# Performance work log

Measured on AMD Instinct MI355X. Metric: run time of the kernel, lower is better.

Reference implementation:

```python
import jax, jax.numpy as jnp
import numpy as np

N_NODES = 50000
IN_F = 512
OUT_F = 512
N_EDGES = 1600000
DROP_P = 0.5
NEG_SLOPE = 0.01  # torch LeakyReLU default


def leaky_relu(x):
    return jnp.where(x >= 0, x, NEG_SLOPE * x)


def setup_inputs() -> dict:
    key = jax.random.key(0)
    k1, k2, k3, k4, k5, k6 = jax.random.split(key, 6)
    x = jax.random.normal(k1, (N_NODES, IN_F), dtype=jnp.float32)
    W = jax.random.normal(k2, (OUT_F, IN_F), dtype=jnp.float32) * (1.0 / np.sqrt(IN_F))
    # inverted dropout mask: bernoulli(keep)/keep, keep = 1 - p
    keep = 1.0 - DROP_P
    drop_mask = (jax.random.uniform(k3, (N_NODES, IN_F)) < keep).astype(jnp.float32) / keep
    adj_vals = jax.random.uniform(k4, (N_EDGES,), dtype=jnp.float32)
    adj_rows = jax.random.randint(k5, (N_EDGES,), 0, N_NODES, dtype=jnp.int32)
    adj_cols = jax.random.randint(k6, (N_EDGES,), 0, N_NODES, dtype=jnp.int32)
    return {"x": x, "W": W, "drop_mask": drop_mask, "adj_vals": adj_vals,
            "adj_rows": adj_rows, "adj_cols": adj_cols}


def reference(x, W, drop_mask, adj_vals, adj_rows, adj_cols):
    # support = Linear(dropout(x)); Linear weight is [out, in] (torch convention)
    support = jnp.einsum('ni,oi->no', x * drop_mask, W)  # [N, out]
    h = leaky_relu(support)
    # sparse adj @ h: out[r] += v * h[c]
    msgs = adj_vals[:, None] * h[adj_cols]               # [E, out]
    agg = jax.ops.segment_sum(msgs, adj_rows, num_segments=N_NODES)
    return leaky_relu(agg)
```

## Files before the change

kernel.cpp:

```cpp
#include <hip/hip_runtime.h>

#define NROWS 50000
#define NFEAT 512
#define NEDGE 1600000
#define SLOPE 0.01f

typedef unsigned short u16;
typedef __attribute__((ext_vector_type(8))) short short8;
typedef __attribute__((ext_vector_type(4))) float f32x4;
typedef __attribute__((ext_vector_type(8))) unsigned short u16x8;

__device__ __forceinline__ u16 f2bf(float f) {
  unsigned u = __float_as_uint(f);
  u += 0x7fffu + ((u >> 16) & 1u);
  return (u16)(u >> 16);
}
__device__ __forceinline__ float lrelu(float v) { return v >= 0.f ? v : SLOPE * v; }

__device__ __forceinline__ void gload_lds16(const u16* g, u16* l) {
  __builtin_amdgcn_global_load_lds((const __attribute__((address_space(1))) void*)g,
                                   (__attribute__((address_space(3))) void*)l, 16, 0, 0);
}

__global__ void prep_kernel(const float* __restrict__ x, const float* __restrict__ m,
                            u16* __restrict__ xd, const float* __restrict__ w,
                            u16* __restrict__ wb, const int* __restrict__ rows,
                            int* __restrict__ counts) {
  const int stride = gridDim.x * blockDim.x;
  const int tid0 = blockIdx.x * blockDim.x + threadIdx.x;
  for (int i = tid0; i < (NROWS * NFEAT) / 8; i += stride) {
    size_t b = (size_t)i * 2;
    float4 a0 = ((const float4*)x)[b], a1 = ((const float4*)x)[b + 1];
    float4 m0 = ((const float4*)m)[b], m1 = ((const float4*)m)[b + 1];
    u16x8 o;
    o[0] = f2bf(a0.x * m0.x); o[1] = f2bf(a0.y * m0.y);
    o[2] = f2bf(a0.z * m0.z); o[3] = f2bf(a0.w * m0.w);
    o[4] = f2bf(a1.x * m1.x); o[5] = f2bf(a1.y * m1.y);
    o[6] = f2bf(a1.z * m1.z); o[7] = f2bf(a1.w * m1.w);
    *(u16x8*)(xd + (size_t)i * 8) = o;
  }
  for (int i = tid0; i < (NFEAT * NFEAT) / 8; i += stride) {
    size_t b = (size_t)i * 2;
    float4 a0 = ((const float4*)w)[b], a1 = ((const float4*)w)[b + 1];
    u16x8 o;
    o[0] = f2bf(a0.x); o[1] = f2bf(a0.y); o[2] = f2bf(a0.z); o[3] = f2bf(a0.w);
    o[4] = f2bf(a1.x); o[5] = f2bf(a1.y); o[6] = f2bf(a1.z); o[7] = f2bf(a1.w);
    *(u16x8*)(wb + (size_t)i * 8) = o;
  }
  for (int i = tid0; i < NEDGE / 4; i += stride) {
    int4 r4 = ((const int4*)rows)[i];
    atomicAdd(&counts[r4.x], 1);
    atomicAdd(&counts[r4.y], 1);
    atomicAdd(&counts[r4.z], 1);
    atomicAdd(&counts[r4.w], 1);
  }
}

__global__ void scan_kernel(const int* __restrict__ counts, int* __restrict__ offs) {
  __shared__ int wpre[17];
  const int t = threadIdx.x;
  const int lane = t & 63, w = t >> 6;
  const int beg = t * 64;
  int4 c4[16];
  int s = 0;
  if (beg < NROWS) {
#pragma unroll
    for (int g = 0; g < 16; ++g) {
      int idx = beg + g * 4;
      if (idx < NROWS) {
        c4[g] = ((const int4*)counts)[idx >> 2];
        s += c4[g].x + c4[g].y + c4[g].z + c4[g].w;
      }
    }
  }
  int inc = s;
#pragma unroll
  for (int d = 1; d < 64; d <<= 1) {
    int u = __shfl_up(inc, d);
    if (lane >= d) inc += u;
  }
  if (lane == 63) wpre[w + 1] = inc;
  __syncthreads();
  if (t == 0) {
    wpre[0] = 0;
    for (int i = 1; i <= 16; ++i) wpre[i] += wpre[i - 1];
    offs[NROWS] = wpre[16];
  }
  __syncthreads();
  int run = wpre[w] + inc - s;
  if (beg < NROWS) {
#pragma unroll
    for (int g = 0; g < 16; ++g) {
      int idx = beg + g * 4;
      if (idx < NROWS) {
        int4 o;
        o.x = run; run += c4[g].x;
        o.y = run; run += c4[g].y;
        o.z = run; run += c4[g].z;
        o.w = run; run += c4[g].w;
        ((int4*)offs)[idx >> 2] = o;
      }
    }
  }
}

__global__ void scatter_kernel(const float* __restrict__ vals, const int* __restrict__ rows,
                               const int* __restrict__ cols, const int* __restrict__ offs,
                               int* __restrict__ cursor, int2* __restrict__ svc) {
  int e0 = (blockIdx.x * blockDim.x + threadIdx.x) * 4;
  if (e0 >= NEDGE) return;
  int4 r4 = *(const int4*)(rows + e0);
  int4 c4 = *(const int4*)(cols + e0);
  float4 v4 = *(const float4*)(vals + e0);
  int rr[4] = {r4.x, r4.y, r4.z, r4.w};
  int cc[4] = {c4.x, c4.y, c4.z, c4.w};
  float vv[4] = {v4.x, v4.y, v4.z, v4.w};
#pragma unroll
  for (int j = 0; j < 4; ++j) {
    int p = offs[rr[j]] + atomicAdd(&cursor[rr[j]], 1);
    int2 q;
    q.x = __float_as_int(vv[j]);
    q.y = cc[j];
    svc[p] = q;
  }
}

__global__ __launch_bounds__(256) void gemm_kernel(const u16* __restrict__ xd,
                                                   const u16* __restrict__ wb,
                                                   unsigned char* __restrict__ hq,
                                                   float* __restrict__ scaleg) {
  __shared__ __align__(16) u16 lAB[2 * 128 * 64];
  __shared__ float wmax[2][128];
  __shared__ float rinv[128];
  u16* lA = lAB;
  u16* lB = lAB + 128 * 64;
  const int tid = threadIdx.x;
  const int lane = tid & 63;
  const int wid = tid >> 6;
  const int wm = wid >> 1, wn = wid & 1;
  const int bx = blockIdx.x;
  const int tm = bx >> 2;
  const int tn = bx & 3;
  const long rowBase = (long)tm * 128;

  f32x4 acc[4][4] = {};

  const int sl8 = lane >> 3;
  const int scol = ((lane & 7) ^ sl8) * 8;
  const int rsel = lane & 15, kgrp = (lane >> 4) * 8;

  for (int k0 = 0; k0 < 512; k0 += 64) {
    __syncthreads();
#pragma unroll
    for (int c = 0; c < 4; ++c) {
      int rbase = wid * 32 + c * 8;
      long gr = rowBase + rbase + sl8;
      if (gr > NROWS - 1) gr = NROWS - 1;
      gload_lds16(xd + gr * 512 + k0 + scol, lA + rbase * 64);
      gload_lds16(wb + ((long)tn * 128 + rbase + sl8) * 512 + k0 + scol, lB + rbase * 64);
    }
    __syncthreads();
    short8 a[4][2], b[4][2];
#pragma unroll
    for (int m = 0; m < 4; ++m) {
      int ar = wm * 64 + m * 16 + rsel;
      const u16* base = lA + ar * 64;
      int sw = (ar & 7) << 3;
      a[m][0] = *(const short8*)(base + (kgrp ^ sw));
      a[m][1] = *(const short8*)(base + ((32 + kgrp) ^ sw));
    }
#pragma unroll
    for (int n = 0; n < 4; ++n) {
      int br = wn * 64 + n * 16 + rsel;
      const u16* base = lB + br * 64;
      int sw = (br & 7) << 3;
      b[n][0] = *(const short8*)(base + (kgrp ^ sw));
      b[n][1] = *(const short8*)(base + ((32 + kgrp) ^ sw));
    }
#pragma unroll
    for (int kk = 0; kk < 2; ++kk)
#pragma unroll
      for (int m = 0; m < 4; ++m)
#pragma unroll
        for (int n = 0; n < 4; ++n)
          acc[m][n] = __builtin_amdgcn_mfma_f32_16x16x32_bf16(a[m][kk], b[n][kk], acc[m][n], 0, 0, 0);
  }

  const int crow = (lane >> 4) * 4;
  const int ccol = lane & 15;

  float pm[4][4];
#pragma unroll
  for (int m = 0; m < 4; ++m)
#pragma unroll
    for (int r2 = 0; r2 < 4; ++r2) {
      float mx = 0.f;
#pragma unroll
      for (int n = 0; n < 4; ++n) mx = fmaxf(mx, fabsf(lrelu(acc[m][n][r2])));
      pm[m][r2] = mx;
    }
#pragma unroll
  for (int d = 1; d < 16; d <<= 1)
#pragma unroll
    for (int m = 0; m < 4; ++m)
#pragma unroll
      for (int r2 = 0; r2 < 4; ++r2) pm[m][r2] = fmaxf(pm[m][r2], __shfl_xor(pm[m][r2], d));
  if ((lane & 15) == 0) {
#pragma unroll
    for (int m = 0; m < 4; ++m)
#pragma unroll
      for (int r2 = 0; r2 < 4; ++r2) wmax[wn][wm * 64 + m * 16 + crow + r2] = pm[m][r2];
  }
  __syncthreads();
  if (tid < 128) {
    float rm = fmaxf(wmax[0][tid], wmax[1][tid]);
    float s = rm > 0.f ? rm * (1.f / 127.f) : 1.f;
    rinv[tid] = rm > 0.f ? 127.f / rm : 0.f;
    long gr = rowBase + tid;
    if (gr < NROWS) scaleg[gr * 4 + tn] = s;
  }
  __syncthreads();

  unsigned char* lT = (unsigned char*)lAB;
#pragma unroll
  for (int m = 0; m < 4; ++m) {
    int row0 = wm * 64 + m * 16 + crow;
    float ri0 = rinv[row0], ri1 = rinv[row0 + 1], ri2 = rinv[row0 + 2], ri3 = rinv[row0 + 3];
#pragma unroll
    for (int n = 0; n < 4; ++n) {
      int col = wn * 64 + n * 16 + ccol;
      float q0 = rintf(lrelu(acc[m][n][0]) * ri0);
      float q1 = rintf(lrelu(acc[m][n][1]) * ri1);
      float q2 = rintf(lrelu(acc[m][n][2]) * ri2);
      float q3 = rintf(lrelu(acc[m][n][3]) * ri3);
      int i0 = min(127, max(-127, (int)q0));
      int i1 = min(127, max(-127, (int)q1));
      int i2 = min(127, max(-127, (int)q2));
      int i3 = min(127, max(-127, (int)q3));
      unsigned pk = (i0 & 0xff) | ((i1 & 0xff) << 8) | ((i2 & 0xff) << 16) | ((i3 & 0xff) << 24);
#pragma unroll
      for (int r2 = 0; r2 < 4; ++r2) {
        int row = row0 + r2;
        lT[row * 128 + (col ^ ((row & 7) << 4))] = (unsigned char)(pk >> (8 * r2));
      }
    }
  }
  __syncthreads();
  {
    const int row = tid >> 1, seg = tid & 1;
    long gr = rowBase + row;
    if (gr < NROWS) {
      unsigned char* dst = hq + gr * 512 + tn * 128;
#pragma unroll
      for (int j = 0; j < 4; ++j) {
        int s = seg * 4 + j;
        int4 vv = *(const int4*)(lT + row * 128 + ((s ^ (row & 7)) << 4));
        *(int4*)(dst + s * 16) = vv;
      }
    }
  }
}

__global__ __launch_bounds__(256) void aggregate_kernel(const unsigned char* __restrict__ hq,
                                                        const float* __restrict__ scaleg,
                                                        const int2* __restrict__ svc,
                                                        const int* __restrict__ offs,
                                                        float* __restrict__ out) {
  const int lane = threadIdx.x & 63;
  const int wid = threadIdx.x >> 6;
  const int p = blockIdx.x / 12500;
  const int r = (blockIdx.x % 12500) * 4 + wid;
  if (r >= NROWS) return;
  const int beg = offs[r], end = offs[r + 1];
  const int grp = p * 2 + (lane >> 5);
  float a0 = 0.f, a1 = 0.f, a2 = 0.f, a3 = 0.f;
  const unsigned char* hp = hq + p * 256 + lane * 4;
  int2 cb[8], nb[8];
  const int ng = (end - beg) >> 3;
  if (ng > 0) {
#pragma unroll
    for (int k = 0; k < 8; ++k) cb[k] = svc[beg + k];
  }
  for (int g = 0; g < ng; ++g) {
    if (g + 1 < ng) {
#pragma unroll
      for (int k = 0; k < 8; ++k) nb[k] = svc[beg + (g + 1) * 8 + k];
    }
#pragma unroll
    for (int k = 0; k < 8; ++k) {
      float v = __int_as_float(cb[k].x);
      size_t c = (size_t)cb[k].y;
      float vs = v * scaleg[c * 4 + grp];
      unsigned q = *(const unsigned*)(hp + c * 512);
      a0 += vs * (float)(signed char)(q);
      a1 += vs * (float)(signed char)(q >> 8);
      a2 += vs * (float)(signed char)(q >> 16);
      a3 += vs * (float)(signed char)(q >> 24);
    }
    if (g + 1 < ng) {
#pragma unroll
      for (int k = 0; k < 8; ++k) cb[k] = nb[k];
    }
  }
  for (int e = beg + ng * 8; e < end; ++e) {
    int2 q2 = svc[e];
    float v = __int_as_float(q2.x);
    size_t c = (size_t)q2.y;
    float vs = v * scaleg[c * 4 + grp];
    unsigned q = *(const unsigned*)(hp + c * 512);
    a0 += vs * (float)(signed char)(q);
    a1 += vs * (float)(signed char)(q >> 8);
    a2 += vs * (float)(signed char)(q >> 16);
    a3 += vs * (float)(signed char)(q >> 24);
  }
  float4 o;
  o.x = lrelu(a0); o.y = lrelu(a1); o.z = lrelu(a2); o.w = lrelu(a3);
  *(float4*)(out + (size_t)r * NFEAT + p * 256 + lane * 4) = o;
}

extern "C" void kernel_launch(void* const* d_in, const int* in_sizes, int n_in,
                              void* d_out, int out_size, void* d_ws, size_t ws_size,
                              hipStream_t stream) {
  const float* x = (const float*)d_in[0];
  const float* W = (const float*)d_in[1];
  const float* mask = (const float*)d_in[2];
  const float* vals = (const float*)d_in[3];
  const int* rows = (const int*)d_in[4];
  const int* cols = (const int*)d_in[5];
  float* out = (float*)d_out;
  char* ws = (char*)d_ws;

  const size_t o_xd = 0;
  const size_t o_hq = o_xd + 51200000;
  const size_t o_wb = o_hq + 25600000;
  const size_t o_scale = o_wb + 524288;
  const size_t o_counts = o_scale + 800000;
  const size_t o_cursor = o_counts + 200000;
  const size_t o_offs = o_cursor + 200000;
  const size_t o_svc = o_offs + 200064;

  u16* xd = (u16*)(ws + o_xd);
  unsigned char* hq = (unsigned char*)(ws + o_hq);
  u16* wb = (u16*)(ws + o_wb);
  float* scaleg = (float*)(ws + o_scale);
  int* counts = (int*)(ws + o_counts);
  int* cursor = (int*)(ws + o_cursor);
  int* offs = (int*)(ws + o_offs);
  int2* svc = (int2*)(ws + o_svc);

  hipMemsetAsync(counts, 0, 400000, stream);

  prep_kernel<<<2048, 256, 0, stream>>>(x, mask, xd, W, wb, rows, counts);
  scan_kernel<<<1, 1024, 0, stream>>>(counts, offs);
  scatter_kernel<<<1563, 256, 0, stream>>>(vals, rows, cols, offs, cursor, svc);
  gemm_kernel<<<391 * 4, 256, 0, stream>>>(xd, wb, hq, scaleg);
  aggregate_kernel<<<25000, 256, 0, stream>>>(hq, scaleg, svc, offs, out);
}
```

Measured before the change: 423.7 us.

## Pack edge list into 32-bit words and aggregate full rows in one pass

Scatter now stores each edge as a 16-bit column index plus a bf16 value in one 32-bit word, halving the sorted edge list. The aggregate kernel processes all 512 features of a row per wavefront with 8-byte int8 gathers, so the edge list and scales are read once instead of twice. The GEMM block index is remapped so consecutive tiles land on the same XCD. Edge weights lose precision to bf16, and the index packing relies on fewer than 65536 nodes.

```diff
diff --git a/kernel.cpp b/kernel.cpp
--- a/kernel.cpp
+++ b/kernel.cpp
@@ -106,7 +106,7 @@
 
 __global__ void scatter_kernel(const float* __restrict__ vals, const int* __restrict__ rows,
                                const int* __restrict__ cols, const int* __restrict__ offs,
-                               int* __restrict__ cursor, int2* __restrict__ svc) {
+                               int* __restrict__ cursor, unsigned* __restrict__ svc) {
   int e0 = (blockIdx.x * blockDim.x + threadIdx.x) * 4;
   if (e0 >= NEDGE) return;
   int4 r4 = *(const int4*)(rows + e0);
@@ -118,10 +118,7 @@
 #pragma unroll
   for (int j = 0; j < 4; ++j) {
     int p = offs[rr[j]] + atomicAdd(&cursor[rr[j]], 1);
-    int2 q;
-    q.x = __float_as_int(vv[j]);
-    q.y = cc[j];
-    svc[p] = q;
+    svc[p] = ((unsigned)cc[j] << 16) | (unsigned)f2bf(vv[j]);
   }
 }
 
@@ -138,9 +135,11 @@
   const int lane = tid & 63;
   const int wid = tid >> 6;
   const int wm = wid >> 1, wn = wid & 1;
-  const int bx = blockIdx.x;
-  const int tm = bx >> 2;
-  const int tn = bx & 3;
+  const int bx0 = blockIdx.x;
+  const int xcd = bx0 & 7, idx = bx0 >> 3;
+  const int wg = (xcd < 4 ? xcd * 196 : 784 + (xcd - 4) * 195) + idx;
+  const int tm = wg >> 2;
+  const int tn = wg & 3;
   const long rowBase = (long)tm * 128;
 
   f32x4 acc[4][4] = {};
@@ -263,19 +262,18 @@
 
 __global__ __launch_bounds__(256) void aggregate_kernel(const unsigned char* __restrict__ hq,
                                                         const float* __restrict__ scaleg,
-                                                        const int2* __restrict__ svc,
+                                                        const unsigned* __restrict__ svc,
                                                         const int* __restrict__ offs,
                                                         float* __restrict__ out) {
   const int lane = threadIdx.x & 63;
   const int wid = threadIdx.x >> 6;
-  const int p = blockIdx.x / 12500;
-  const int r = (blockIdx.x % 12500) * 4 + wid;
+  const int r = blockIdx.x * 4 + wid;
   if (r >= NROWS) return;
   const int beg = offs[r], end = offs[r + 1];
-  const int grp = p * 2 + (lane >> 5);
-  float a0 = 0.f, a1 = 0.f, a2 = 0.f, a3 = 0.f;
-  const unsigned char* hp = hq + p * 256 + lane * 4;
-  int2 cb[8], nb[8];
+  const int grp = lane >> 4;
+  float a[8] = {};
+  const unsigned char* hp = hq + lane * 8;
+  unsigned cb[8], nb[8];
   const int ng = (end - beg) >> 3;
   if (ng > 0) {
 #pragma unroll
@@ -288,14 +286,18 @@
     }
 #pragma unroll
     for (int k = 0; k < 8; ++k) {
-      float v = __int_as_float(cb[k].x);
-      size_t c = (size_t)cb[k].y;
+      float v = __uint_as_float(cb[k] << 16);
+      size_t c = (size_t)(cb[k] >> 16);
       float vs = v * scaleg[c * 4 + grp];
-      unsigned q = *(const unsigned*)(hp + c * 512);
-      a0 += vs * (float)(signed char)(q);
-      a1 += vs * (float)(signed char)(q >> 8);
-      a2 += vs * (float)(signed char)(q >> 16);
-      a3 += vs * (float)(signed char)(q >> 24);
+      uint2 q = *(const uint2*)(hp + c * 512);
+      a[0] += vs * (float)(signed char)(q.x);
+      a[1] += vs * (float)(signed char)(q.x >> 8);
+      a[2] += vs * (float)(signed char)(q.x >> 16);
+      a[3] += vs * (float)(signed char)(q.x >> 24);
+      a[4] += vs * (float)(signed char)(q.y);
+      a[5] += vs * (float)(signed char)(q.y >> 8);
+      a[6] += vs * (float)(signed char)(q.y >> 16);
+      a[7] += vs * (float)(signed char)(q.y >> 24);
     }
     if (g + 1 < ng) {
 #pragma unroll
@@ -303,19 +305,26 @@
     }
   }
   for (int e = beg + ng * 8; e < end; ++e) {
-    int2 q2 = svc[e];
-    float v = __int_as_float(q2.x);
-    size_t c = (size_t)q2.y;
+    unsigned q2 = svc[e];
+    float v = __uint_as_float(q2 << 16);
+    size_t c = (size_t)(q2 >> 16);
     float vs = v * scaleg[c * 4 + grp];
-    unsigned q = *(const unsigned*)(hp + c * 512);
-    a0 += vs * (float)(signed char)(q);
-    a1 += vs * (float)(signed char)(q >> 8);
-    a2 += vs * (float)(signed char)(q >> 16);
-    a3 += vs * (float)(signed char)(q >> 24);
-  }
-  float4 o;
-  o.x = lrelu(a0); o.y = lrelu(a1); o.z = lrelu(a2); o.w = lrelu(a3);
-  *(float4*)(out + (size_t)r * NFEAT + p * 256 + lane * 4) = o;
+    uint2 q = *(const uint2*)(hp + c * 512);
+    a[0] += vs * (float)(signed char)(q.x);
+    a[1] += vs * (float)(signed char)(q.x >> 8);
+    a[2] += vs * (float)(signed char)(q.x >> 16);
+    a[3] += vs * (float)(signed char)(q.x >> 24);
+    a[4] += vs * (float)(signed char)(q.y);
+    a[5] += vs * (float)(signed char)(q.y >> 8);
+    a[6] += vs * (float)(signed char)(q.y >> 16);
+    a[7] += vs * (float)(signed char)(q.y >> 24);
+  }
+  float* op = out + (size_t)r * NFEAT + lane * 8;
+  float4 o0, o1;
+  o0.x = lrelu(a[0]); o0.y = lrelu(a[1]); o0.z = lrelu(a[2]); o0.w = lrelu(a[3]);
+  o1.x = lrelu(a[4]); o1.y = lrelu(a[5]); o1.z = lrelu(a[6]); o1.w = lrelu(a[7]);
+  *(float4*)op = o0;
+  *(float4*)(op + 4) = o1;
 }
 
 extern "C" void kernel_launch(void* const* d_in, const int* in_sizes, int n_in,
@@ -346,7 +355,7 @@
   int* counts = (int*)(ws + o_counts);
   int* cursor = (int*)(ws + o_cursor);
   int* offs = (int*)(ws + o_offs);
-  int2* svc = (int2*)(ws + o_svc);
+  unsigned* svc = (unsigned*)(ws + o_svc);
 
   hipMemsetAsync(counts, 0, 400000, stream);
 
@@ -354,5 +363,5 @@
   scan_kernel<<<1, 1024, 0, stream>>>(counts, offs);
   scatter_kernel<<<1563, 256, 0, stream>>>(vals, rows, cols, offs, cursor, svc);
   gemm_kernel<<<391 * 4, 256, 0, stream>>>(xd, wb, hq, scaleg);
-  aggregate_kernel<<<25000, 256, 0, stream>>>(hq, scaleg, svc, offs, out);
-}
+  aggregate_kernel<<<12500, 256, 0, stream>>>(hq, scaleg, svc, offs, out);
+}
```

New measurement: 405.8 us. -4.2%, faster.
